# Kernel optimization log

Measured on AMD Instinct MI355X. Metric: run time of the kernel, lower is better.

## Reference

```python
import jax, jax.numpy as jnp
import numpy as np

ALPHA = 1.0
EPS = 1e-8  # torch cosine_similarity default eps


def setup_inputs() -> dict:
    key = jax.random.key(0)
    k1, k2 = jax.random.split(key)
    N, D, J, C = 2048, 64, 20, 3
    predictions = jax.random.normal(k1, (N, D), dtype=jnp.float32)
    data = jax.random.normal(k2, (N, J, C), dtype=jnp.float32)
    return {"predictions": predictions, "data": data}


def reference(predictions, data):
    N = predictions.shape[0]
    # Strict upper triangle i<j. The original loop also includes (i,i) pairs for
    # i < N-1, but those contribute exactly 0 to the loss (dist=0, dis=sqrt(sum(1-1))=0);
    # they only affect the normalizer num = N*(N+1)//2 - 1, which we keep.
    mask = jnp.triu(jnp.ones((N, N), dtype=bool), k=1)

    # Pairwise L2 distances via Gram matrix (avoids [N,N,D] intermediate).
    sq_norms = jnp.sum(predictions * predictions, axis=1)          # [N]
    gram = predictions @ predictions.T                              # [N,N]
    d2 = jnp.maximum(sq_norms[:, None] + sq_norms[None, :] - 2.0 * gram, 0.0)
    dist = jnp.sqrt(jnp.where(mask, d2, 1.0)) * mask                # [N,N], safe sqrt

    # Pairwise bone distance: per-joint cosine similarity over the C axis.
    norms = jnp.sqrt(jnp.sum(data * data, axis=2))                  # [N,J]
    dots = jnp.einsum('ikc,jkc->ijk', data, data)                   # [N,N,J]
    denom = jnp.maximum(norms[:, None, :] * norms[None, :, :], EPS)
    cos = jnp.clip(dots / denom, -1.0, 1.0)
    s = jnp.sum(1.0 - cos * cos, axis=2)                            # [N,N]
    dis = jnp.sqrt(jnp.where(mask, s, 1.0)) * mask                  # safe sqrt

    num = N * (N + 1) // 2 - 1                                      # loop pair count
    loss = jnp.sum(jnp.abs(ALPHA * dist - dis)) / num
    return loss
```

## Files before the change

kernel.cpp:

```cpp
#include <hip/hip_runtime.h>

#define N_PTS 2048
#define D_DIM 64
#define N_J   20
#define KD    192
#define LDSW  200
#define T_TILES 32
#define NTILES 528
#define NUM_PAIRS_D 2098175.0

typedef __attribute__((ext_vector_type(8))) short bf16x8;
typedef __attribute__((ext_vector_type(4))) float f32x4;

__device__ inline unsigned short f2bf(float f) {
    union { float f; unsigned int u; } v; v.f = f;
    unsigned int u = v.u;
    return (unsigned short)((u + 0x7FFFu + ((u >> 16) & 1u)) >> 16);
}
__device__ inline unsigned int pack2(float lo, float hi) {
    return (unsigned int)f2bf(lo) | ((unsigned int)f2bf(hi) << 16);
}

__global__ __launch_bounds__(256, 3)
void pairloss_kernel(const float* __restrict__ pred,
                     const float* __restrict__ data,
                     float* __restrict__ partials) {
    __shared__ unsigned short Ash[64 * LDSW];
    __shared__ unsigned short Bsh[64 * LDSW];
    __shared__ float sqA[64], sqB[64], wsum[4];

    const int t = blockIdx.x;
    int ib = (int)((65.0f - sqrtf(4225.0f - 8.0f * (float)t)) * 0.5f);
    if (ib > T_TILES - 1) ib = T_TILES - 1;
    if (ib < 0) ib = 0;
    #define TRI_OFF(i) ((i) * T_TILES - ((i) * ((i) - 1)) / 2)
    while (ib > 0 && t < TRI_OFF(ib)) --ib;
    while (ib < T_TILES - 1 && t >= TRI_OFF(ib + 1)) ++ib;
    const int jb = ib + (t - TRI_OFF(ib));

    const int tid = threadIdx.x;

    {
        const int half = tid >> 7;
        const int r    = (tid >> 1) & 63;
        const int h    = tid & 1;
        const int grow = (half ? jb : ib) * 64 + r;
        unsigned short* __restrict__ sh = half ? Bsh : Ash;

        const float4* __restrict__ p4 = (const float4*)&pred[grow * D_DIM + h * 32];
        float s = 0.f;
        #pragma unroll
        for (int q = 0; q < 4; ++q) {
            const float4 v0 = p4[2 * q];
            const float4 v1 = p4[2 * q + 1];
            s += v0.x * v0.x + v0.y * v0.y + v0.z * v0.z + v0.w * v0.w
               + v1.x * v1.x + v1.y * v1.y + v1.z * v1.z + v1.w * v1.w;
            uint4 u;
            u.x = pack2(v0.x, v0.y);
            u.y = pack2(v0.z, v0.w);
            u.z = pack2(v1.x, v1.y);
            u.w = pack2(v1.z, v1.w);
            *(uint4*)&sh[r * LDSW + h * 32 + q * 8] = u;
        }
        s += __shfl_xor(s, 1);
        if (h == 0) (half ? sqB : sqA)[r] = s;

        const float2* __restrict__ d2 = (const float2*)&data[grow * (N_J * 3) + h * 30];
        float buf[30];
        #pragma unroll
        for (int q = 0; q < 15; ++q) {
            const float2 v = d2[q];
            buf[2 * q] = v.x; buf[2 * q + 1] = v.y;
        }
        unsigned int wreg[32];
        const float s2 = 1.4142135623730951f;
        #pragma unroll
        for (int jj = 0; jj < 10; ++jj) {
            float x = buf[3 * jj], y = buf[3 * jj + 1], z = buf[3 * jj + 2];
            const float inv = rsqrtf(fmaxf(x * x + y * y + z * z, 1e-30f));
            x *= inv; y *= inv; z *= inv;
            wreg[3 * jj + 0] = pack2(x * x, y * y);
            wreg[3 * jj + 1] = pack2(z * z, s2 * x * y);
            wreg[3 * jj + 2] = pack2(s2 * x * z, s2 * y * z);
        }
        wreg[30] = 0u; wreg[31] = 0u;
        #pragma unroll
        for (int q = 0; q < 8; ++q) {
            uint4 u;
            u.x = wreg[4 * q + 0]; u.y = wreg[4 * q + 1];
            u.z = wreg[4 * q + 2]; u.w = wreg[4 * q + 3];
            *(uint4*)&sh[r * LDSW + D_DIM + h * 64 + q * 8] = u;
        }
    }
    __syncthreads();

    const int w  = tid >> 6;
    const int l  = tid & 63;
    const int lr = l & 15;
    const int kg = l >> 4;

    f32x4 accP[4], accW[4];
    #pragma unroll
    for (int c4 = 0; c4 < 4; ++c4) {
        accP[c4] = (f32x4){0.f, 0.f, 0.f, 0.f};
        accW[c4] = (f32x4){0.f, 0.f, 0.f, 0.f};
    }

    const unsigned short* Abase = &Ash[(w * 16 + lr) * LDSW + kg * 8];
    const unsigned short* Bbase = &Bsh[lr * LDSW + kg * 8];

    __builtin_amdgcn_s_setprio(1);
    #pragma unroll
    for (int ks = 0; ks < 6; ++ks) {
        const bf16x8 af = *(const bf16x8*)(Abase + ks * 32);
        #pragma unroll
        for (int c4 = 0; c4 < 4; ++c4) {
            const bf16x8 bf = *(const bf16x8*)(Bbase + c4 * 16 * LDSW + ks * 32);
            if (ks < 2)
                accP[c4] = __builtin_amdgcn_mfma_f32_16x16x32_bf16(af, bf, accP[c4], 0, 0, 0);
            else
                accW[c4] = __builtin_amdgcn_mfma_f32_16x16x32_bf16(af, bf, accW[c4], 0, 0, 0);
        }
    }
    __builtin_amdgcn_s_setprio(0);

    const int ri0 = w * 16 + kg * 4;
    const int i0  = ib * 64 + ri0;
    float sqi[4];
    #pragma unroll
    for (int r = 0; r < 4; ++r) sqi[r] = sqA[ri0 + r];

    float local = 0.0f;
    #pragma unroll
    for (int c4 = 0; c4 < 4; ++c4) {
        const int jl = c4 * 16 + lr;
        const int j  = jb * 64 + jl;
        const float sqj = sqB[jl];
        #pragma unroll
        for (int r = 0; r < 4; ++r) {
            const int i = i0 + r;
            if (j > i) {
                const float d2   = fmaxf(sqi[r] + sqj - 2.0f * accP[c4][r], 0.0f);
                const float dist = sqrtf(d2);
                const float s    = fmaxf((float)N_J - accW[c4][r], 0.0f);
                local += fabsf(dist - sqrtf(s));
            }
        }
    }

    #pragma unroll
    for (int off = 32; off > 0; off >>= 1) local += __shfl_down(local, off);
    if (l == 0) wsum[w] = local;
    __syncthreads();
    if (tid == 0) partials[blockIdx.x] = wsum[0] + wsum[1] + wsum[2] + wsum[3];
}

__global__ __launch_bounds__(256)
void finalize_kernel(const float* __restrict__ partials, float* __restrict__ out) {
    double s = 0.0;
    for (int i = threadIdx.x; i < NTILES; i += 256) s += (double)partials[i];
    #pragma unroll
    for (int off = 32; off > 0; off >>= 1) s += __shfl_down(s, off);
    __shared__ double sh4[4];
    if ((threadIdx.x & 63) == 0) sh4[threadIdx.x >> 6] = s;
    __syncthreads();
    if (threadIdx.x == 0)
        out[0] = (float)((sh4[0] + sh4[1] + sh4[2] + sh4[3]) / NUM_PAIRS_D);
}

extern "C" void kernel_launch(void* const* d_in, const int* in_sizes, int n_in,
                              void* d_out, int out_size, void* d_ws, size_t ws_size,
                              hipStream_t stream) {
    const float* pred = (const float*)d_in[0];
    const float* data = (const float*)d_in[1];
    float* out = (float*)d_out;

    float* partials = (float*)d_ws;

    pairloss_kernel<<<NTILES, 256, 0, stream>>>(pred, data, partials);
    finalize_kernel<<<1, 256, 0, stream>>>(partials, out);
}
```

Baseline: 18.16 us.

## Precompute bf16 features once and fuse final reduction via last-block atomic

Adds a precompute kernel that converts predictions and normalized bone features to packed bf16 rows, along with squared norms, once per point. The pair kernel then only copies these rows into LDS, avoiding the conversion being redone for the same rows by up to 32 tiles each. The separate finalize launch is replaced with a last-block-done atomic counter that performs the final double reduction. The counter relies on modulo wraparound, so it works across repeated calls without being reset. It adds a workspace round trip through global memory plus an atomic and fences.

```diff
diff --git a/kernel.cpp b/kernel.cpp
--- a/kernel.cpp
+++ b/kernel.cpp
@@ -4,6 +4,7 @@
 #define D_DIM 64
 #define N_J   20
 #define KD    192
+#define KDW   96
 #define LDSW  200
 #define T_TILES 32
 #define NTILES 528
@@ -21,13 +22,55 @@
     return (unsigned int)f2bf(lo) | ((unsigned int)f2bf(hi) << 16);
 }
 
+__global__ __launch_bounds__(256)
+void precompute_kernel(const float* __restrict__ pred,
+                       const float* __restrict__ data,
+                       unsigned int* __restrict__ Gb,
+                       float* __restrict__ sq) {
+    const int team = threadIdx.x >> 6;
+    const int t    = threadIdx.x & 63;
+    const int i    = blockIdx.x * 4 + team;
+    unsigned int* __restrict__ grow = Gb + i * KDW;
+
+    if (t < 32) {
+        const float2 v = *(const float2*)&pred[i * D_DIM + 2 * t];
+        grow[t] = pack2(v.x, v.y);
+        float s = v.x * v.x + v.y * v.y;
+        #pragma unroll
+        for (int off = 16; off > 0; off >>= 1) s += __shfl_down(s, off, 32);
+        if (t == 0) sq[i] = s;
+    } else {
+        const int jj = t - 32;
+        if (jj < N_J) {
+            float x = data[(i * N_J + jj) * 3 + 0];
+            float y = data[(i * N_J + jj) * 3 + 1];
+            float z = data[(i * N_J + jj) * 3 + 2];
+            const float inv = rsqrtf(fmaxf(x * x + y * y + z * z, 1e-30f));
+            x *= inv; y *= inv; z *= inv;
+            const float s2 = 1.4142135623730951f;
+            const int dw = (jj < 10) ? (32 + jj * 3) : (64 + (jj - 10) * 3);
+            grow[dw + 0] = pack2(x * x, y * y);
+            grow[dw + 1] = pack2(z * z, s2 * x * y);
+            grow[dw + 2] = pack2(s2 * x * z, s2 * y * z);
+        } else if (jj == 20) {
+            grow[62] = 0u; grow[63] = 0u;
+        } else if (jj == 21) {
+            grow[94] = 0u; grow[95] = 0u;
+        }
+    }
+}
+
 __global__ __launch_bounds__(256, 3)
-void pairloss_kernel(const float* __restrict__ pred,
-                     const float* __restrict__ data,
-                     float* __restrict__ partials) {
+void pairloss_kernel(const unsigned int* __restrict__ Gb,
+                     const float* __restrict__ sq,
+                     float* __restrict__ partials,
+                     unsigned int* __restrict__ counter,
+                     float* __restrict__ out) {
     __shared__ unsigned short Ash[64 * LDSW];
     __shared__ unsigned short Bsh[64 * LDSW];
     __shared__ float sqA[64], sqB[64], wsum[4];
+    __shared__ bool  trig;
+    __shared__ double dsh[4];
 
     const int t = blockIdx.x;
     int ib = (int)((65.0f - sqrtf(4225.0f - 8.0f * (float)t)) * 0.5f);
@@ -41,57 +84,21 @@
     const int tid = threadIdx.x;
 
     {
-        const int half = tid >> 7;
-        const int r    = (tid >> 1) & 63;
-        const int h    = tid & 1;
-        const int grow = (half ? jb : ib) * 64 + r;
-        unsigned short* __restrict__ sh = half ? Bsh : Ash;
-
-        const float4* __restrict__ p4 = (const float4*)&pred[grow * D_DIM + h * 32];
-        float s = 0.f;
+        const uint4* __restrict__ g4 = (const uint4*)Gb;
         #pragma unroll
-        for (int q = 0; q < 4; ++q) {
-            const float4 v0 = p4[2 * q];
-            const float4 v1 = p4[2 * q + 1];
-            s += v0.x * v0.x + v0.y * v0.y + v0.z * v0.z + v0.w * v0.w
-               + v1.x * v1.x + v1.y * v1.y + v1.z * v1.z + v1.w * v1.w;
-            uint4 u;
-            u.x = pack2(v0.x, v0.y);
-            u.y = pack2(v0.z, v0.w);
-            u.z = pack2(v1.x, v1.y);
-            u.w = pack2(v1.z, v1.w);
-            *(uint4*)&sh[r * LDSW + h * 32 + q * 8] = u;
-        }
-        s += __shfl_xor(s, 1);
-        if (h == 0) (half ? sqB : sqA)[r] = s;
-
-        const float2* __restrict__ d2 = (const float2*)&data[grow * (N_J * 3) + h * 30];
-        float buf[30];
-        #pragma unroll
-        for (int q = 0; q < 15; ++q) {
-            const float2 v = d2[q];
-            buf[2 * q] = v.x; buf[2 * q + 1] = v.y;
-        }
-        unsigned int wreg[32];
-        const float s2 = 1.4142135623730951f;
-        #pragma unroll
-        for (int jj = 0; jj < 10; ++jj) {
-            float x = buf[3 * jj], y = buf[3 * jj + 1], z = buf[3 * jj + 2];
-            const float inv = rsqrtf(fmaxf(x * x + y * y + z * z, 1e-30f));
-            x *= inv; y *= inv; z *= inv;
-            wreg[3 * jj + 0] = pack2(x * x, y * y);
-            wreg[3 * jj + 1] = pack2(z * z, s2 * x * y);
-            wreg[3 * jj + 2] = pack2(s2 * x * z, s2 * y * z);
-        }
-        wreg[30] = 0u; wreg[31] = 0u;
-        #pragma unroll
-        for (int q = 0; q < 8; ++q) {
-            uint4 u;
-            u.x = wreg[4 * q + 0]; u.y = wreg[4 * q + 1];
-            u.z = wreg[4 * q + 2]; u.w = wreg[4 * q + 3];
-            *(uint4*)&sh[r * LDSW + D_DIM + h * 64 + q * 8] = u;
+        for (int q = 0; q < 12; ++q) {
+            const int s    = q * 256 + tid;
+            const int sA   = (s < 1536) ? s : (s - 1536);
+            const int r    = (int)(((unsigned)sA * 43691u) >> 20);
+            const int c    = sA - 24 * r;
+            const int gr   = ((s < 1536) ? ib : jb) * 64 + r;
+            const uint4 v  = g4[gr * 24 + c];
+            unsigned short* __restrict__ sh = (s < 1536) ? Ash : Bsh;
+            *(uint4*)&sh[(r * 25 + c) * 8] = v;
         }
     }
+    if (tid < 64)        sqA[tid]      = sq[ib * 64 + tid];
+    else if (tid < 128)  sqB[tid - 64] = sq[jb * 64 + (tid - 64)];
     __syncthreads();
 
     const int w  = tid >> 6;
@@ -152,20 +159,26 @@
     for (int off = 32; off > 0; off >>= 1) local += __shfl_down(local, off);
     if (l == 0) wsum[w] = local;
     __syncthreads();
-    if (tid == 0) partials[blockIdx.x] = wsum[0] + wsum[1] + wsum[2] + wsum[3];
-}
 
-__global__ __launch_bounds__(256)
-void finalize_kernel(const float* __restrict__ partials, float* __restrict__ out) {
-    double s = 0.0;
-    for (int i = threadIdx.x; i < NTILES; i += 256) s += (double)partials[i];
-    #pragma unroll
-    for (int off = 32; off > 0; off >>= 1) s += __shfl_down(s, off);
-    __shared__ double sh4[4];
-    if ((threadIdx.x & 63) == 0) sh4[threadIdx.x >> 6] = s;
+    if (tid == 0) {
+        partials[blockIdx.x] = wsum[0] + wsum[1] + wsum[2] + wsum[3];
+        __threadfence();
+        const unsigned int old = atomicAdd(counter, 1u);
+        trig = ((old % (unsigned)NTILES) == (unsigned)(NTILES - 1));
+    }
     __syncthreads();
-    if (threadIdx.x == 0)
-        out[0] = (float)((sh4[0] + sh4[1] + sh4[2] + sh4[3]) / NUM_PAIRS_D);
+    if (trig) {
+        __threadfence();
+        double s = 0.0;
+        for (int idx = tid; idx < NTILES; idx += 256)
+            s += (double)((volatile const float*)partials)[idx];
+        #pragma unroll
+        for (int off = 32; off > 0; off >>= 1) s += __shfl_down(s, off);
+        if ((tid & 63) == 0) dsh[tid >> 6] = s;
+        __syncthreads();
+        if (tid == 0)
+            out[0] = (float)((dsh[0] + dsh[1] + dsh[2] + dsh[3]) / NUM_PAIRS_D);
+    }
 }
 
 extern "C" void kernel_launch(void* const* d_in, const int* in_sizes, int n_in,
@@ -175,8 +188,12 @@
     const float* data = (const float*)d_in[1];
     float* out = (float*)d_out;
 
-    float* partials = (float*)d_ws;
+    char* ws = (char*)d_ws;
+    unsigned int* Gb      = (unsigned int*)ws;
+    float*        sq      = (float*)(ws + 786432);
+    float*        partials= (float*)(ws + 786432 + 8192);
+    unsigned int* counter = (unsigned int*)(ws + 786432 + 8192 + 2112);
 
-    pairloss_kernel<<<NTILES, 256, 0, stream>>>(pred, data, partials);
-    finalize_kernel<<<1, 256, 0, stream>>>(partials, out);
+    precompute_kernel<<<N_PTS / 4, 256, 0, stream>>>(pred, data, Gb, sq);
+    pairloss_kernel<<<NTILES, 256, 0, stream>>>(Gb, sq, partials, counter, out);
 }
```

New measurement: 25.97 us. 1.43x slower.
